# Kernel tuning notes

Hardware: AMD Instinct MI355X
Metric: run time of the kernel (lower is better)

## Reference

```python
import jax, jax.numpy as jnp
import numpy as np

B, T, D, SD, CHUNK = 4, 4096, 1024, 512, 32


def setup_inputs() -> dict:
    key = jax.random.key(0)
    ks = jax.random.split(key, 6)
    sc_in = 1.0 / np.sqrt(D)
    sc_out = 1.0 / np.sqrt(2 * SD)
    return {
        "x": jax.random.normal(ks[0], (B, T, D), jnp.float32),
        "Wt": jax.random.normal(ks[1], (D, SD), jnp.float32) * sc_in,
        "bt": jnp.zeros((SD,), jnp.float32),
        "Wr": jax.random.normal(ks[2], (D, SD), jnp.float32) * sc_in,
        "br": jnp.zeros((SD,), jnp.float32),
        "Wi": jax.random.normal(ks[3], (D, 2 * SD), jnp.float32) * sc_in,
        "bi": jnp.zeros((2 * SD,), jnp.float32),
        "Wo": jax.random.normal(ks[4], (2 * SD, D), jnp.float32) * sc_out,
        "bo": jnp.zeros((D,), jnp.float32),
        "gamma": jnp.ones((D,), jnp.float32),
        "beta": jnp.zeros((D,), jnp.float32),
    }


def _rotation_scan(theta, retain, b_r, b_i, chunk):
    # theta/retain/b_*: [B, T, d]. Chunked linear recurrence h[t]=a[t]*h[t-1]+b[t]
    # with a[t] = retain[t]*e^{i theta[t]}, done in log-magnitude/angle space.
    Bsz, Tlen, d = theta.shape
    K = min(chunk, Tlen)
    n = Tlen // K  # T assumed divisible by K (4096 / 32)
    resh = lambda a: a.reshape(Bsz, n, K, d).transpose(1, 0, 2, 3)  # [n,B,K,d]
    th_c, rt_c, br_c, bi_c = resh(theta), resh(retain), resh(b_r), resh(b_i)

    def step(carry, xs):
        h_r, h_i = carry  # [B, d]
        th, rt, cb_r, cb_i = xs  # [B, K, d]
        cum_log_mag = jnp.cumsum(jnp.log(jnp.clip(rt, 1e-6, None)), axis=1)
        cum_mag = jnp.exp(cum_log_mag)
        cum_th = jnp.cumsum(th, axis=1)
        cum_cos = jnp.cos(cum_th)
        cum_sin = jnp.sin(cum_th)
        cum_a_r = cum_mag * cum_cos
        cum_a_i = cum_mag * cum_sin
        inv_mag = 1.0 / jnp.clip(cum_mag, 1e-8, None)
        inv_r = inv_mag * cum_cos          # cos(-t) = cos(t)
        inv_i = -inv_mag * cum_sin         # sin(-t) = -sin(t)
        scaled_b_r = inv_r * cb_r - inv_i * cb_i
        scaled_b_i = inv_r * cb_i + inv_i * cb_r
        cum_b_r = jnp.cumsum(scaled_b_r, axis=1)
        cum_b_i = jnp.cumsum(scaled_b_i, axis=1)
        tot_r = h_r[:, None] + cum_b_r
        tot_i = h_i[:, None] + cum_b_i
        ch_r = cum_a_r * tot_r - cum_a_i * tot_i
        ch_i = cum_a_r * tot_i + cum_a_i * tot_r
        return (ch_r[:, -1], ch_i[:, -1]), (ch_r, ch_i)

    h0 = (jnp.zeros((Bsz, d), theta.dtype), jnp.zeros((Bsz, d), theta.dtype))
    _, (out_r, out_i) = jax.lax.scan(step, h0, (th_c, rt_c, br_c, bi_c))
    back = lambda a: a.transpose(1, 0, 2, 3).reshape(Bsz, Tlen, d)
    return back(out_r), back(out_i)


def reference(x, Wt, bt, Wr, br, Wi, bi, Wo, bo, gamma, beta):
    d = Wt.shape[1]
    theta = x @ Wt + bt                       # [B,T,d]
    retain = jax.nn.sigmoid(x @ Wr + br)      # [B,T,d]
    inp = x @ Wi + bi                          # [B,T,2d]
    inp_r, inp_i = inp[..., :d], inp[..., d:]
    drive = 1.0 - retain
    out_r, out_i = _rotation_scan(theta, retain, drive * inp_r, drive * inp_i, CHUNK)
    out = jnp.concatenate([out_r, out_i], axis=-1)  # [B,T,2d]
    y = x + out @ Wo + bo
    mu = jnp.mean(y, axis=-1, keepdims=True)
    var = jnp.var(y, axis=-1, keepdims=True)
    return (y - mu) / jnp.sqrt(var + 1e-5) * gamma + beta
```

## Files before the change

kernel.cpp:

```cpp
#include <hip/hip_runtime.h>
#include <cstdint>


typedef __bf16 bf16x8 __attribute__((ext_vector_type(8)));
typedef float  f32x4  __attribute__((ext_vector_type(4)));
typedef ushort u16x8  __attribute__((ext_vector_type(8)));

#define AS1 __attribute__((address_space(1)))
#define AS3 __attribute__((address_space(3)))

__device__ __forceinline__ void gload16(const void* g, void* l) {
  __builtin_amdgcn_global_load_lds((const AS1 void*)g, (AS3 void*)l, 16, 0, 0);
}

__device__ __forceinline__ ushort f2bf(float f) {
  union { float f; uint32_t u; } v; v.f = f;
  uint32_t u = v.u;
  uint32_t r = u + 0x7FFFu + ((u >> 16) & 1u);
  return (ushort)(r >> 16);
}
__device__ __forceinline__ float bf2f(ushort u) {
  union { uint32_t x; float f; } v; v.x = (uint32_t)u << 16; return v.f;
}

__global__ __launch_bounds__(256) void tconv_all(const float* __restrict__ Wt,
                                                 const float* __restrict__ Wr,
                                                 const float* __restrict__ Wi,
                                                 const float* __restrict__ Wo,
                                                 ushort* __restrict__ wcat,
                                                 ushort* __restrict__ wot) {
  const int z = blockIdx.z;
  if (z < 2 && blockIdx.x >= 16) return;
  const float* src = (z == 0) ? Wt : (z == 1) ? Wr : (z == 2) ? Wi : Wo;
  const int C = (z < 2) ? 512 : 1024;
  const int row_off = (z == 0) ? 0 : (z == 1) ? 512 : (z == 2) ? 1024 : 0;
  ushort* dst = (z == 3) ? wot : wcat;

  __shared__ float tile[32][33];
  int tx = threadIdx.x, ty = threadIdx.y;
  int rb = blockIdx.y * 32, cb = blockIdx.x * 32;
#pragma unroll
  for (int yy = 0; yy < 4; ++yy) {
    int r = rb + ty + yy * 8;
    tile[ty + yy * 8][tx] = src[(size_t)r * C + cb + tx];
  }
  __syncthreads();
#pragma unroll
  for (int yy = 0; yy < 4; ++yy) {
    int c = cb + ty + yy * 8;
    dst[(size_t)(row_off + c) * 1024 + rb + tx] = f2bf(tile[tx][ty + yy * 8]);
  }
}

__global__ __launch_bounds__(256) void pack_bias(const float* __restrict__ bt,
                                                 const float* __restrict__ br,
                                                 const float* __restrict__ bi,
                                                 float* __restrict__ bcat) {
  int i = blockIdx.x * 256 + threadIdx.x;
  bcat[i] = (i < 512) ? bt[i] : (i < 1024 ? br[i - 512] : bi[i - 1024]);
}

__global__ __launch_bounds__(256) void xconv(const float4* __restrict__ src,
                                             ushort* __restrict__ dst, int n4) {
  int i = blockIdx.x * 256 + threadIdx.x;
  if (i < n4) {
    float4 v = src[i];
    ushort4 o;
    o.x = f2bf(v.x); o.y = f2bf(v.y); o.z = f2bf(v.z); o.w = f2bf(v.w);
    *(ushort4*)(dst + (size_t)i * 4) = o;
  }
}

__global__ __launch_bounds__(512, 2) void gemm256(const ushort* __restrict__ A,
                                                  const ushort* __restrict__ Bt,
                                                  ushort* __restrict__ C,
                                                  const float* __restrict__ bias,
                                                  int M, int N, int K, int nbn) {
  __shared__ alignas(16) ushort smem[65536];
  ushort* const As0 = smem;
  ushort* const Bs0 = smem + 2 * 256 * 64;

  const int cpx = gridDim.x >> 3;
  const int wg = ((int)blockIdx.x & 7) * cpx + ((int)blockIdx.x >> 3);
  const int bm = wg / nbn, bn = wg % nbn;

  const int t = threadIdx.x;
  const int l = t & 63, w = t >> 6;
  const int wm = w >> 2, wn = w & 3;
  const int r = l & 15, kq = l >> 4;

  const size_t a0 = (size_t)bm * 256 * K;
  const size_t b0 = (size_t)bn * 256 * K;

  const int srow = t >> 3;
  const int sslot = (t & 7) ^ (srow & 7);
  const ushort* gA = A + a0 + (size_t)srow * K + sslot * 8;
  const ushort* gB = Bt + b0 + (size_t)srow * K + sslot * 8;
  const int lboff = w * 1024 + l * 16;

  f32x4 acc[8][4] = {};
  const int NKT = K >> 6;

#define STGA(buf, kt, u) \
  gload16(gA + (size_t)((u) * 64) * K + (size_t)(kt) * 64, \
          (char*)(As0 + (buf) * 256 * 64) + (u) * 8192 + lboff)
#define STGB(buf, kt, u) \
  gload16(gB + (size_t)((u) * 64) * K + (size_t)(kt) * 64, \
          (char*)(Bs0 + (buf) * 256 * 64) + (u) * 8192 + lboff)

#define QUAD(ph)                                                               \
  do {                                                                         \
    _Pragma("unroll")                                                          \
    for (int ii = 0; ii < 2; ++ii) {                                           \
      bf16x8 aF[2];                                                            \
      const int rowa = wm * 128 + ((ph) * 2 + ii) * 16 + r;                    \
      _Pragma("unroll")                                                        \
      for (int ks = 0; ks < 2; ++ks) {                                         \
        const int j = (ks * 4 + kq) ^ (r & 7);                                 \
        aF[ks] = *(const bf16x8*)&pA[rowa * 64 + j * 8];                       \
      }                                                                        \
      __builtin_amdgcn_s_setprio(1);                                           \
      _Pragma("unroll")                                                        \
      for (int jn = 0; jn < 4; ++jn)                                           \
        _Pragma("unroll")                                                      \
        for (int ks = 0; ks < 2; ++ks)                                         \
          acc[(ph) * 2 + ii][jn] = __builtin_amdgcn_mfma_f32_16x16x32_bf16(    \
              aF[ks], bF[jn][ks], acc[(ph) * 2 + ii][jn], 0, 0, 0);            \
      __builtin_amdgcn_s_setprio(0);                                           \
    }                                                                          \
  } while (0)

  STGB(0, 0, 0); STGB(0, 0, 1); STGB(0, 0, 2); STGB(0, 0, 3);
  STGA(0, 0, 0); STGA(0, 0, 2); STGA(0, 0, 1); STGA(0, 0, 3);

  for (int kt = 0; kt < NKT; ++kt) {
    const int cur = kt & 1, nxt = cur ^ 1;
    const bool hn = (kt + 1 < NKT);
    const ushort* pA = As0 + cur * 256 * 64;
    const ushort* pB = Bs0 + cur * 256 * 64;

    if (hn) { STGB(nxt, kt + 1, 0); STGB(nxt, kt + 1, 1); }
    if (hn) asm volatile("s_waitcnt vmcnt(2)" ::: "memory");
    else    asm volatile("s_waitcnt vmcnt(0)" ::: "memory");
    __builtin_amdgcn_s_barrier();
    asm volatile("" ::: "memory");
    bf16x8 bF[4][2];
#pragma unroll
    for (int jn = 0; jn < 4; ++jn) {
      const int rowb = wn * 64 + jn * 16 + r;
#pragma unroll
      for (int ks = 0; ks < 2; ++ks) {
        const int j = (ks * 4 + kq) ^ (r & 7);
        bF[jn][ks] = *(const bf16x8*)&pB[rowb * 64 + j * 8];
      }
    }
    QUAD(0);
    if (hn) { STGB(nxt, kt + 1, 2); STGB(nxt, kt + 1, 3); }
    QUAD(1);
    bf16x8 aFn[2][2];
#pragma unroll
    for (int ii = 0; ii < 2; ++ii) {
      const int rowa = wm * 128 + (4 + ii) * 16 + r;
#pragma unroll
      for (int ks = 0; ks < 2; ++ks) {
        const int j = (ks * 4 + kq) ^ (r & 7);
        aFn[ii][ks] = *(const bf16x8*)&pA[rowa * 64 + j * 8];
      }
    }
    if (hn) { STGA(nxt, kt + 1, 0); STGA(nxt, kt + 1, 2); }
    asm volatile("" ::: "memory");
    __builtin_amdgcn_s_barrier();
    __builtin_amdgcn_s_setprio(1);
#pragma unroll
    for (int ii = 0; ii < 2; ++ii)
#pragma unroll
      for (int jn = 0; jn < 4; ++jn)
#pragma unroll
        for (int ks = 0; ks < 2; ++ks)
          acc[4 + ii][jn] = __builtin_amdgcn_mfma_f32_16x16x32_bf16(
              aFn[ii][ks], bF[jn][ks], acc[4 + ii][jn], 0, 0, 0);
    __builtin_amdgcn_s_setprio(0);
    if (hn) { STGA(nxt, kt + 1, 1); STGA(nxt, kt + 1, 3); }
    QUAD(3);
  }
#undef STGA
#undef STGB
#undef QUAD

  asm volatile("s_waitcnt lgkmcnt(0) vmcnt(0)" ::: "memory");
  __builtin_amdgcn_s_barrier();

  const int q4 = (l >> 4) * 4;
  float bvj[4];
#pragma unroll
  for (int jn = 0; jn < 4; ++jn) {
    const int col = wn * 64 + jn * 16 + r;
    bvj[jn] = bias ? bias[bn * 256 + col] : 0.f;
  }
#pragma unroll
  for (int i = 0; i < 8; ++i) {
#pragma unroll
    for (int jn = 0; jn < 4; ++jn) {
      const int col = wn * 64 + jn * 16 + r;
      const int chunk = col >> 3;
#pragma unroll
      for (int q = 0; q < 4; ++q) {
        const int rowl = wm * 128 + i * 16 + q4 + q;
        const int pch = chunk ^ (rowl & 7);
        smem[rowl * 256 + pch * 8 + (col & 7)] = f2bf(acc[i][jn][q] + bvj[jn]);
      }
    }
  }
  __builtin_amdgcn_s_barrier();

  const int rrow0 = t >> 5;
  const int rch = t & 31;
#pragma unroll
  for (int p = 0; p < 16; ++p) {
    const int rowl = p * 16 + rrow0;
    const int pch = rch ^ (rowl & 7);
    u16x8 vv = *(const u16x8*)&smem[rowl * 256 + pch * 8];
    const size_t grow = (size_t)(bm * 256 + rowl);
    *(u16x8*)&C[grow * N + bn * 256 + rch * 8] = vv;
  }
}

__global__ __launch_bounds__(256) void scan_k1(const ushort* __restrict__ lin,
                                               float4* __restrict__ agg) {
  int bd = blockIdx.x * 256 + threadIdx.x;
  int c  = blockIdx.y;
  int b  = bd >> 9, d = bd & 511;
  const ushort* base = lin + ((size_t)b * 4096 + (size_t)c * 32) * 2048;
  float cth = 0.f, cbr = 0.f, cbi = 0.f;
  float cm = 1.f, cs = 1.f, sn = 0.f;
#pragma unroll 4
  for (int t = 0; t < 32; ++t) {
    const ushort* row = base + (size_t)t * 2048;
    float th = bf2f(row[d]);
    float z  = bf2f(row[512 + d]);
    float ir = bf2f(row[1024 + d]);
    float ii = bf2f(row[1536 + d]);
    float rt = __fdividef(1.f, 1.f + __expf(-z));
    cm *= fmaxf(rt, 1e-6f);
    cth += th;
    float s_, c_;
    __sincosf(cth, &s_, &c_);
    float im = __fdividef(1.f, fmaxf(cm, 1e-8f));
    float invr = im * c_, invi = -im * s_;
    float drive = 1.f - rt;
    float br_ = drive * ir, bi_ = drive * ii;
    cbr += invr * br_ - invi * bi_;
    cbi += invr * bi_ + invi * br_;
    cs = c_; sn = s_;
  }
  agg[(size_t)c * 2048 + bd] = make_float4(cm * cs, cm * sn, cbr, cbi);
}

__global__ __launch_bounds__(256) void scan_k2(const float4* __restrict__ agg,
                                               float2* __restrict__ h0) {
  int bd = blockIdx.x * 256 + threadIdx.x;
  float hr = 0.f, hi = 0.f;
  for (int cg = 0; cg < 16; ++cg) {
    float4 a[8];
#pragma unroll
    for (int u = 0; u < 8; ++u) a[u] = agg[(size_t)(cg * 8 + u) * 2048 + bd];
#pragma unroll
    for (int u = 0; u < 8; ++u) {
      h0[(size_t)(cg * 8 + u) * 2048 + bd] = make_float2(hr, hi);
      float tr = hr + a[u].z, ti = hi + a[u].w;
      hr = a[u].x * tr - a[u].y * ti;
      hi = a[u].x * ti + a[u].y * tr;
    }
  }
}

__global__ __launch_bounds__(256) void scan_k3(const ushort* __restrict__ lin,
                                               const float2* __restrict__ h0,
                                               ushort* __restrict__ outb) {
  int bd = blockIdx.x * 256 + threadIdx.x;
  int c  = blockIdx.y;
  int b  = bd >> 9, d = bd & 511;
  const ushort* base = lin + ((size_t)b * 4096 + (size_t)c * 32) * 2048;
  float2 h = h0[(size_t)c * 2048 + bd];
  float cth = 0.f, cbr = 0.f, cbi = 0.f, cm = 1.f;
#pragma unroll 4
  for (int t = 0; t < 32; ++t) {
    const ushort* row = base + (size_t)t * 2048;
    float th = bf2f(row[d]);
    float z  = bf2f(row[512 + d]);
    float ir = bf2f(row[1024 + d]);
    float ii = bf2f(row[1536 + d]);
    float rt = __fdividef(1.f, 1.f + __expf(-z));
    cm *= fmaxf(rt, 1e-6f);
    cth += th;
    float s_, c_;
    __sincosf(cth, &s_, &c_);
    float im = __fdividef(1.f, fmaxf(cm, 1e-8f));
    float invr = im * c_, invi = -im * s_;
    float drive = 1.f - rt;
    float br_ = drive * ir, bi_ = drive * ii;
    cbr += invr * br_ - invi * bi_;
    cbi += invr * bi_ + invi * br_;
    float ar = cm * c_, ai = cm * s_;
    float tr = h.x + cbr, ti = h.y + cbi;
    float orr = ar * tr - ai * ti;
    float oii = ar * ti + ai * tr;
    size_t rowo = ((size_t)b * 4096 + (size_t)c * 32 + t) * 1024;
    outb[rowo + d] = f2bf(orr);
    outb[rowo + 512 + d] = f2bf(oii);
  }
}

__global__ __launch_bounds__(256) void ln_k(const ushort* __restrict__ yb,
                                            const ushort* __restrict__ xb,
                                            const float* __restrict__ gamma,
                                            const float* __restrict__ beta,
                                            float* __restrict__ out) {
  const int lane = threadIdx.x & 63;
  const size_t row = (size_t)blockIdx.x * 4 + (threadIdx.x >> 6);
  const ushort* yr = yb + row * 1024;
  const ushort* xr = xb + row * 1024;
  float v[4][4];
  float s = 0.f, s2 = 0.f;
#pragma unroll
  for (int q = 0; q < 4; ++q) {
    ushort4 uy = *(const ushort4*)(yr + q * 256 + lane * 4);
    ushort4 ux = *(const ushort4*)(xr + q * 256 + lane * 4);
    v[q][0] = bf2f(uy.x) + bf2f(ux.x);
    v[q][1] = bf2f(uy.y) + bf2f(ux.y);
    v[q][2] = bf2f(uy.z) + bf2f(ux.z);
    v[q][3] = bf2f(uy.w) + bf2f(ux.w);
#pragma unroll
    for (int j = 0; j < 4; ++j) { s += v[q][j]; s2 += v[q][j] * v[q][j]; }
  }
#pragma unroll
  for (int off = 32; off > 0; off >>= 1) {
    s  += __shfl_xor(s, off);
    s2 += __shfl_xor(s2, off);
  }
  const float mu = s * (1.f / 1024.f);
  const float rstd = rsqrtf(s2 * (1.f / 1024.f) - mu * mu + 1e-5f);
#pragma unroll
  for (int q = 0; q < 4; ++q) {
    float4 gv = *(const float4*)(gamma + q * 256 + lane * 4);
    float4 bv = *(const float4*)(beta + q * 256 + lane * 4);
    float4 o;
    o.x = (v[q][0] - mu) * rstd * gv.x + bv.x;
    o.y = (v[q][1] - mu) * rstd * gv.y + bv.y;
    o.z = (v[q][2] - mu) * rstd * gv.z + bv.z;
    o.w = (v[q][3] - mu) * rstd * gv.w + bv.w;
    *(float4*)(out + row * 1024 + q * 256 + lane * 4) = o;
  }
}

extern "C" void kernel_launch(void* const* d_in, const int* in_sizes, int n_in,
                              void* d_out, int out_size, void* d_ws, size_t ws_size,
                              hipStream_t stream) {
  (void)in_sizes; (void)n_in; (void)out_size; (void)ws_size;
  const float* x  = (const float*)d_in[0];
  const float* Wt = (const float*)d_in[1];
  const float* bt = (const float*)d_in[2];
  const float* Wr = (const float*)d_in[3];
  const float* br = (const float*)d_in[4];
  const float* Wi = (const float*)d_in[5];
  const float* bi = (const float*)d_in[6];
  const float* Wo = (const float*)d_in[7];
  const float* bo = (const float*)d_in[8];
  const float* gamma = (const float*)d_in[9];
  const float* beta  = (const float*)d_in[10];

  char* ws = (char*)d_ws;
  ushort* wcat_t = (ushort*)(ws);
  ushort* wo_t   = (ushort*)(ws + ((size_t)4  << 20));
  float*  bcat   = (float*) (ws + ((size_t)6  << 20));
  float4* agg    = (float4*)(ws + ((size_t)8  << 20));
  float2* h0     = (float2*)(ws + ((size_t)12 << 20));
  ushort* xb     = (ushort*)(ws + ((size_t)16 << 20));
  ushort* outb   = (ushort*)(ws + ((size_t)48 << 20));
  ushort* linb   = (ushort*)(ws + ((size_t)80 << 20));
  ushort* yb     = (ushort*)(ws + ((size_t)80 << 20));

  tconv_all<<<dim3(32, 32, 4), dim3(32, 8), 0, stream>>>(Wt, Wr, Wi, Wo, wcat_t, wo_t);
  pack_bias<<<8, 256, 0, stream>>>(bt, br, bi, bcat);
  xconv<<<16384, 256, 0, stream>>>((const float4*)x, xb, 4194304);

  gemm256<<<512, 512, 0, stream>>>(xb, wcat_t, linb, bcat, 16384, 2048, 1024, 8);

  scan_k1<<<dim3(8, 128), 256, 0, stream>>>(linb, agg);
  scan_k2<<<8, 256, 0, stream>>>(agg, h0);
  scan_k3<<<dim3(8, 128), 256, 0, stream>>>(linb, h0, outb);

  gemm256<<<256, 512, 0, stream>>>(outb, wo_t, yb, bo, 16384, 1024, 1024, 4);

  ln_k<<<4096, 256, 0, stream>>>(yb, xb, gamma, beta, (float*)d_out);
}
```

Baseline: 199.3 us.

## Fuse fp32-to-bf16 conversion of x into first GEMM's A-tile loader

Removes the standalone xconv kernel and the bf16 copy of x. The input-projection GEMM now loads fp32 A tiles into registers, converts them to bf16 and writes them to LDS, with the loads for the next k-tile issued before the barrier. The LayerNorm residual reads x in fp32 directly. This saves a full read and write pass over x, but it doubles A-side global traffic inside the GEMM and replaces the async global-to-LDS loads with register staging and explicit vmcnt waits, which adds register pressure.

New measurement: 198.6 us. No clear change (-0.4%).

```diff
diff --git a/kernel.cpp b/kernel.cpp
--- a/kernel.cpp
+++ b/kernel.cpp
@@ -21,6 +21,12 @@
 }
 __device__ __forceinline__ float bf2f(ushort u) {
   union { uint32_t x; float f; } v; v.x = (uint32_t)u << 16; return v.f;
+}
+__device__ __forceinline__ u16x8 cvt8(float4 a, float4 b) {
+  u16x8 o;
+  o[0] = f2bf(a.x); o[1] = f2bf(a.y); o[2] = f2bf(a.z); o[3] = f2bf(a.w);
+  o[4] = f2bf(b.x); o[5] = f2bf(b.y); o[6] = f2bf(b.z); o[7] = f2bf(b.w);
+  return o;
 }
 
 __global__ __launch_bounds__(256) void tconv_all(const float* __restrict__ Wt,
@@ -60,18 +66,8 @@
   bcat[i] = (i < 512) ? bt[i] : (i < 1024 ? br[i - 512] : bi[i - 1024]);
 }
 
-__global__ __launch_bounds__(256) void xconv(const float4* __restrict__ src,
-                                             ushort* __restrict__ dst, int n4) {
-  int i = blockIdx.x * 256 + threadIdx.x;
-  if (i < n4) {
-    float4 v = src[i];
-    ushort4 o;
-    o.x = f2bf(v.x); o.y = f2bf(v.y); o.z = f2bf(v.z); o.w = f2bf(v.w);
-    *(ushort4*)(dst + (size_t)i * 4) = o;
-  }
-}
-
-__global__ __launch_bounds__(512, 2) void gemm256(const ushort* __restrict__ A,
+template <bool AF32>
+__global__ __launch_bounds__(512, 2) void gemm256(const void* __restrict__ Aptr,
                                                   const ushort* __restrict__ Bt,
                                                   ushort* __restrict__ C,
                                                   const float* __restrict__ bias,
@@ -94,19 +90,26 @@
 
   const int srow = t >> 3;
   const int sslot = (t & 7) ^ (srow & 7);
-  const ushort* gA = A + a0 + (size_t)srow * K + sslot * 8;
+  const ushort* gA16 = (const ushort*)Aptr + a0 + (size_t)srow * K + sslot * 8;
+  const float*  gAf  = (const float*)Aptr + a0 + (size_t)srow * K + sslot * 8;
   const ushort* gB = Bt + b0 + (size_t)srow * K + sslot * 8;
   const int lboff = w * 1024 + l * 16;
 
   f32x4 acc[8][4] = {};
   const int NKT = K >> 6;
+  float4 areg[4][2];
 
 #define STGA(buf, kt, u) \
-  gload16(gA + (size_t)((u) * 64) * K + (size_t)(kt) * 64, \
+  gload16(gA16 + (size_t)((u) * 64) * K + (size_t)(kt) * 64, \
           (char*)(As0 + (buf) * 256 * 64) + (u) * 8192 + lboff)
 #define STGB(buf, kt, u) \
   gload16(gB + (size_t)((u) * 64) * K + (size_t)(kt) * 64, \
           (char*)(Bs0 + (buf) * 256 * 64) + (u) * 8192 + lboff)
+#define ALOAD(kt, u) \
+  do { const float* gs_ = gAf + (size_t)((u) * 64) * K + (size_t)(kt) * 64; \
+       areg[u][0] = *(const float4*)gs_; areg[u][1] = *(const float4*)(gs_ + 4); } while (0)
+#define AWRITE(buf, u) \
+  *(u16x8*)((char*)(As0 + (buf) * 256 * 64) + (u) * 8192 + lboff) = cvt8(areg[u][0], areg[u][1])
 
 #define QUAD(ph)                                                               \
   do {                                                                         \
@@ -131,7 +134,14 @@
   } while (0)
 
   STGB(0, 0, 0); STGB(0, 0, 1); STGB(0, 0, 2); STGB(0, 0, 3);
-  STGA(0, 0, 0); STGA(0, 0, 2); STGA(0, 0, 1); STGA(0, 0, 3);
+  if constexpr (AF32) {
+#pragma unroll
+    for (int u = 0; u < 4; ++u) ALOAD(0, u);
+#pragma unroll
+    for (int u = 0; u < 4; ++u) AWRITE(0, u);
+  } else {
+    STGA(0, 0, 0); STGA(0, 0, 2); STGA(0, 0, 1); STGA(0, 0, 3);
+  }
 
   for (int kt = 0; kt < NKT; ++kt) {
     const int cur = kt & 1, nxt = cur ^ 1;
@@ -140,8 +150,18 @@
     const ushort* pB = Bs0 + cur * 256 * 64;
 
     if (hn) { STGB(nxt, kt + 1, 0); STGB(nxt, kt + 1, 1); }
-    if (hn) asm volatile("s_waitcnt vmcnt(2)" ::: "memory");
-    else    asm volatile("s_waitcnt vmcnt(0)" ::: "memory");
+    if constexpr (AF32) {
+      if (hn) {
+#pragma unroll
+        for (int u = 0; u < 4; ++u) ALOAD(kt + 1, u);
+        asm volatile("s_waitcnt vmcnt(10) lgkmcnt(0)" ::: "memory");
+      } else {
+        asm volatile("s_waitcnt vmcnt(0) lgkmcnt(0)" ::: "memory");
+      }
+    } else {
+      if (hn) asm volatile("s_waitcnt vmcnt(2)" ::: "memory");
+      else    asm volatile("s_waitcnt vmcnt(0)" ::: "memory");
+    }
     __builtin_amdgcn_s_barrier();
     asm volatile("" ::: "memory");
     bf16x8 bF[4][2];
@@ -167,7 +187,10 @@
         aFn[ii][ks] = *(const bf16x8*)&pA[rowa * 64 + j * 8];
       }
     }
-    if (hn) { STGA(nxt, kt + 1, 0); STGA(nxt, kt + 1, 2); }
+    if (hn) {
+      if constexpr (AF32) { AWRITE(nxt, 0); AWRITE(nxt, 1); }
+      else                { STGA(nxt, kt + 1, 0); STGA(nxt, kt + 1, 2); }
+    }
     asm volatile("" ::: "memory");
     __builtin_amdgcn_s_barrier();
     __builtin_amdgcn_s_setprio(1);
@@ -180,11 +203,16 @@
           acc[4 + ii][jn] = __builtin_amdgcn_mfma_f32_16x16x32_bf16(
               aFn[ii][ks], bF[jn][ks], acc[4 + ii][jn], 0, 0, 0);
     __builtin_amdgcn_s_setprio(0);
-    if (hn) { STGA(nxt, kt + 1, 1); STGA(nxt, kt + 1, 3); }
+    if (hn) {
+      if constexpr (AF32) { AWRITE(nxt, 2); AWRITE(nxt, 3); }
+      else                { STGA(nxt, kt + 1, 1); STGA(nxt, kt + 1, 3); }
+    }
     QUAD(3);
   }
 #undef STGA
 #undef STGB
+#undef ALOAD
+#undef AWRITE
 #undef QUAD
 
   asm volatile("s_waitcnt lgkmcnt(0) vmcnt(0)" ::: "memory");
@@ -312,24 +340,24 @@
 }
 
 __global__ __launch_bounds__(256) void ln_k(const ushort* __restrict__ yb,
-                                            const ushort* __restrict__ xb,
+                                            const float* __restrict__ x,
                                             const float* __restrict__ gamma,
                                             const float* __restrict__ beta,
                                             float* __restrict__ out) {
   const int lane = threadIdx.x & 63;
   const size_t row = (size_t)blockIdx.x * 4 + (threadIdx.x >> 6);
   const ushort* yr = yb + row * 1024;
-  const ushort* xr = xb + row * 1024;
+  const float* xr = x + row * 1024;
   float v[4][4];
   float s = 0.f, s2 = 0.f;
 #pragma unroll
   for (int q = 0; q < 4; ++q) {
     ushort4 uy = *(const ushort4*)(yr + q * 256 + lane * 4);
-    ushort4 ux = *(const ushort4*)(xr + q * 256 + lane * 4);
-    v[q][0] = bf2f(uy.x) + bf2f(ux.x);
-    v[q][1] = bf2f(uy.y) + bf2f(ux.y);
-    v[q][2] = bf2f(uy.z) + bf2f(ux.z);
-    v[q][3] = bf2f(uy.w) + bf2f(ux.w);
+    float4 fx = *(const float4*)(xr + q * 256 + lane * 4);
+    v[q][0] = bf2f(uy.x) + fx.x;
+    v[q][1] = bf2f(uy.y) + fx.y;
+    v[q][2] = bf2f(uy.z) + fx.z;
+    v[q][3] = bf2f(uy.w) + fx.w;
 #pragma unroll
     for (int j = 0; j < 4; ++j) { s += v[q][j]; s2 += v[q][j] * v[q][j]; }
   }
@@ -375,22 +403,20 @@
   float*  bcat   = (float*) (ws + ((size_t)6  << 20));
   float4* agg    = (float4*)(ws + ((size_t)8  << 20));
   float2* h0     = (float2*)(ws + ((size_t)12 << 20));
-  ushort* xb     = (ushort*)(ws + ((size_t)16 << 20));
   ushort* outb   = (ushort*)(ws + ((size_t)48 << 20));
   ushort* linb   = (ushort*)(ws + ((size_t)80 << 20));
   ushort* yb     = (ushort*)(ws + ((size_t)80 << 20));
 
   tconv_all<<<dim3(32, 32, 4), dim3(32, 8), 0, stream>>>(Wt, Wr, Wi, Wo, wcat_t, wo_t);
   pack_bias<<<8, 256, 0, stream>>>(bt, br, bi, bcat);
-  xconv<<<16384, 256, 0, stream>>>((const float4*)x, xb, 4194304);
-
-  gemm256<<<512, 512, 0, stream>>>(xb, wcat_t, linb, bcat, 16384, 2048, 1024, 8);
+
+  gemm256<true><<<512, 512, 0, stream>>>(x, wcat_t, linb, bcat, 16384, 2048, 1024, 8);
 
   scan_k1<<<dim3(8, 128), 256, 0, stream>>>(linb, agg);
   scan_k2<<<8, 256, 0, stream>>>(agg, h0);
   scan_k3<<<dim3(8, 128), 256, 0, stream>>>(linb, h0, outb);
 
-  gemm256<<<256, 512, 0, stream>>>(outb, wo_t, yb, bo, 16384, 1024, 1024, 4);
-
-  ln_k<<<4096, 256, 0, stream>>>(yb, xb, gamma, beta, (float*)d_out);
-}
+  gemm256<false><<<256, 512, 0, stream>>>(outb, wo_t, yb, bo, 16384, 1024, 1024, 4);
+
+  ln_k<<<4096, 256, 0, stream>>>(yb, x, gamma, beta, (float*)d_out);
+}
```
